# Optimization experiments

Measured on AMD Instinct MI355X. Metric: run time of the kernel, lower is better.

The kernel has to match this reference:

```python
import jax, jax.numpy as jnp
import numpy as np

NEG_SLOPE = 0.2  # PyG GATConv default negative_slope


def _gat(x, src, dst, N, W, a_src, a_dst, b, heads, ch, concat):
    # x: [N, F_in]; src/dst: [E] (self-loops already appended)
    h = (x @ W).reshape(N, heads, ch)                      # [N,H,C]
    s = jnp.sum(h * a_src, axis=-1)                        # [N,H]
    d = jnp.sum(h * a_dst, axis=-1)                        # [N,H]
    e = jax.nn.leaky_relu(s[src] + d[dst], NEG_SLOPE)      # [E,H]
    # segment softmax over incoming edges of each dst node
    m = jax.ops.segment_max(e, dst, num_segments=N)        # [N,H]
    ex = jnp.exp(e - m[dst])
    den = jax.ops.segment_sum(ex, dst, num_segments=N)     # [N,H]
    alpha = ex / den[dst]                                  # [E,H]
    out = jax.ops.segment_sum(h[src] * alpha[:, :, None], dst, num_segments=N)  # [N,H,C]
    out = out.reshape(N, heads * ch) if concat else out.mean(axis=1)
    return out + b


def setup_inputs() -> dict:
    key = jax.random.key(0)
    ks = jax.random.split(key, 20)
    N, E, F_in, H, C = 50000, 400000, 64, 4, 128
    x = jax.random.normal(ks[0], (N, F_in), dtype=jnp.float32)
    edge_index = jax.random.randint(ks[1], (2, E), 0, N, dtype=jnp.int64)

    def lin(k, fi, fo):
        return jax.random.normal(k, (fi, fo), dtype=jnp.float32) / np.float32(np.sqrt(fi))

    def att(k, h, c):
        return jax.random.normal(k, (h, c), dtype=jnp.float32) / np.float32(np.sqrt(c))

    return {
        "x": x, "edge_index": edge_index,
        "W1": lin(ks[2], F_in, H * C), "as1": att(ks[3], H, C), "ad1": att(ks[4], H, C), "b1": jnp.zeros((H * C,), jnp.float32),
        "W2": lin(ks[5], H * C, H * C), "as2": att(ks[6], H, C), "ad2": att(ks[7], H, C), "b2": jnp.zeros((H * C,), jnp.float32),
        "W3": lin(ks[8], H * C, C), "as3": att(ks[9], 1, C), "ad3": att(ks[10], 1, C), "b3": jnp.zeros((C,), jnp.float32),
        "cW1": lin(ks[11], C, C // 2), "cb1": jnp.zeros((C // 2,), jnp.float32),
        "cW2": lin(ks[12], C // 2, 2), "cb2": jnp.zeros((2,), jnp.float32),
    }


def reference(x, edge_index, W1, as1, ad1, b1, W2, as2, ad2, b2, W3, as3, ad3, b3, cW1, cb1, cW2, cb2):
    N = x.shape[0]
    loops = jnp.arange(N, dtype=edge_index.dtype)
    src = jnp.concatenate([edge_index[0], loops])
    dst = jnp.concatenate([edge_index[1], loops])
    h = _gat(x, src, dst, N, W1, as1, ad1, b1, 4, 128, True)
    h = jax.nn.relu(h)                         # dropout is identity at eval
    h = _gat(h, src, dst, N, W2, as2, ad2, b2, 4, 128, True)
    h = jax.nn.relu(h)
    h = _gat(h, src, dst, N, W3, as3, ad3, b3, 1, 128, False)
    out = jax.nn.relu(h @ cW1 + cb1) @ cW2 + cb2
    return jax.nn.log_softmax(out, axis=-1)
```

## Files before the change

### kernel.cpp

```cpp
#include <hip/hip_runtime.h>
#include <math.h>

#define NEG_SLOPE 0.2f

typedef __attribute__((ext_vector_type(8))) short short8;
typedef __attribute__((ext_vector_type(4))) float f32x4;
typedef unsigned short ushort_t;
typedef unsigned int u32;
typedef __attribute__((ext_vector_type(8))) unsigned short ushort8;
typedef __attribute__((ext_vector_type(4))) unsigned short ushort4v;

__device__ inline ushort_t f2bf(float f) {
    unsigned int u = __builtin_bit_cast(unsigned int, f);
    u += 0x7fffu + ((u >> 16) & 1u);
    return (ushort_t)(u >> 16);
}
__device__ inline float bf2f(ushort_t u) {
    unsigned int v = ((unsigned int)u) << 16;
    return __builtin_bit_cast(float, v);
}

__device__ inline void gl_lds16(const ushort_t* g, ushort_t* l) {
    __builtin_amdgcn_global_load_lds((const __attribute__((address_space(1))) u32*)g,
                                     (__attribute__((address_space(3))) u32*)l, 16, 0, 0);
}

__device__ inline int xcd_swizzle(int id, int nwg) {
    int q = nwg >> 3, r = nwg & 7;
    int xcd = id & 7, j = id >> 3;
    return (xcd < r ? xcd * (q + 1) : r * (q + 1) + (xcd - r) * q) + j;
}


__global__ void convert_count_kernel(const int* __restrict__ ei, int E, int N,
                                     int* __restrict__ deg,
                                     const float* __restrict__ x, ushort_t* __restrict__ xb, int n4x,
                                     const float* __restrict__ W1, ushort_t* __restrict__ W1t,
                                     const float* __restrict__ W2, ushort_t* __restrict__ W2t,
                                     const float* __restrict__ W3, ushort_t* __restrict__ W3t,
                                     const float* __restrict__ cW1, ushort_t* __restrict__ cW1t,
                                     const float* __restrict__ as1, const float* __restrict__ ad1,
                                     float* __restrict__ W1as, float* __restrict__ W1ad) {
    int i = blockIdx.x * blockDim.x + threadIdx.x;
    if (i < E + N) {
        int d = (i < E) ? ei[E + i] : (i - E);
        atomicAdd(&deg[d], 1);
    }
    if (i < n4x) {
        float4 v = ((const float4*)x)[i];
        ushort4v o;
        o.x = f2bf(v.x); o.y = f2bf(v.y); o.z = f2bf(v.z); o.w = f2bf(v.w);
        ((ushort4v*)xb)[i] = o;
        return;
    }
    int j = i - n4x;
    if (j < 64 * 512) {
        int k = j / 512, nn = j % 512;
        W1t[(size_t)nn * 64 + k] = f2bf(W1[j]);
        return;
    }
    j -= 64 * 512;
    if (j < 512 * 512) {
        int k = j / 512, nn = j % 512;
        W2t[(size_t)nn * 512 + k] = f2bf(W2[j]);
        return;
    }
    j -= 512 * 512;
    if (j < 512 * 128) {
        int k = j / 128, nn = j % 128;
        W3t[(size_t)nn * 512 + k] = f2bf(W3[j]);
        return;
    }
    j -= 512 * 128;
    if (j < 128 * 64) {
        int k = j / 64, nn = j % 64;
        cW1t[(size_t)nn * 128 + k] = f2bf(cW1[j]);
        return;
    }
    j -= 128 * 64;
    if (j < 512) {
        int k = j >> 3;
        int idx = j & 7;
        int h = idx & 3;
        int sel = idx >> 2;
        const float* av = sel ? ad1 : as1;
        float* outw = sel ? W1ad : W1as;
        const float* wrow = W1 + (size_t)k * 512 + h * 128;
        const float* arow = av + h * 128;
        float acc = 0.f;
        for (int c = 0; c < 128; c++) acc += wrow[c] * arow[c];
        outw[k * 4 + h] = acc;
    }
}

__global__ void scan1_kernel(const int* __restrict__ deg, int* __restrict__ rowptr,
                             int* __restrict__ bsum, int N) {
    __shared__ int sdata[256];
    int t = threadIdx.x;
    int base = blockIdx.x * 1024 + t * 4;
    int v[4];
#pragma unroll
    for (int k = 0; k < 4; k++) v[k] = (base + k < N) ? deg[base + k] : 0;
    int s = v[0] + v[1] + v[2] + v[3];
    sdata[t] = s;
    __syncthreads();
    for (int off = 1; off < 256; off <<= 1) {
        int x = (t >= off) ? sdata[t - off] : 0;
        __syncthreads();
        sdata[t] += x;
        __syncthreads();
    }
    int p = sdata[t] - s;
    if (t == 255) bsum[blockIdx.x] = sdata[255];
#pragma unroll
    for (int k = 0; k < 4; k++) {
        if (base + k < N) rowptr[base + k] = p;
        p += v[k];
    }
}

__global__ void scan2_kernel(int* __restrict__ bsum, int* __restrict__ rowptr, int nb, int N) {
    __shared__ int sh[256];
    int t = threadIdx.x;
    int v = (t < nb) ? bsum[t] : 0;
    sh[t] = v;
    __syncthreads();
    for (int off = 1; off < 256; off <<= 1) {
        int x = (t >= off) ? sh[t - off] : 0;
        __syncthreads();
        sh[t] += x;
        __syncthreads();
    }
    if (t < nb) bsum[t] = sh[t] - v;
    if (t == 255) rowptr[N] = sh[255];
}

__global__ void scan3_kernel(const int* __restrict__ bsum, int* __restrict__ rowptr,
                             int* __restrict__ cursor, int N) {
    int i = blockIdx.x * blockDim.x + threadIdx.x;
    if (i < N) {
        int v = rowptr[i] + bsum[i >> 10];
        rowptr[i] = v;
        cursor[i] = v;
    }
}

__global__ void fill_csr_kernel(const int* __restrict__ ei, int E, int N,
                                int* __restrict__ cursor, int* __restrict__ srcS) {
    int e = blockIdx.x * blockDim.x + threadIdx.x;
    if (e >= E + N) return;
    int s, d;
    if (e < E) { s = ei[e]; d = ei[E + e]; }
    else       { s = e - E; d = e - E; }
    int pos = atomicAdd(&cursor[d], 1);
    srcS[pos] = s;
}


__global__ __launch_bounds__(256) void score1_kernel(const ushort_t* __restrict__ xb,
                                                     const float* __restrict__ W1as,
                                                     const float* __restrict__ W1ad,
                                                     float* __restrict__ sOut,
                                                     float* __restrict__ dOut, int N) {
    __shared__ float wa[256];
    __shared__ float wd[256];
    int t = threadIdx.x;
    wa[t] = W1as[t];
    wd[t] = W1ad[t];
    __syncthreads();
    int n = blockIdx.x * 256 + t;
    if (n >= N) return;
    const ushort_t* xr = xb + (size_t)n * 64;
    float s_[4] = {0.f, 0.f, 0.f, 0.f};
    float d_[4] = {0.f, 0.f, 0.f, 0.f};
#pragma unroll
    for (int k8 = 0; k8 < 8; k8++) {
        ushort8 xv = *(const ushort8*)(xr + k8 * 8);
#pragma unroll
        for (int kk = 0; kk < 8; kk++) {
            float xf = bf2f(xv[kk]);
            int k = k8 * 8 + kk;
#pragma unroll
            for (int h = 0; h < 4; h++) {
                s_[h] += xf * wa[k * 4 + h];
                d_[h] += xf * wd[k * 4 + h];
            }
        }
    }
#pragma unroll
    for (int h = 0; h < 4; h++) {
        sOut[(size_t)n * 4 + h] = s_[h];
        dOut[(size_t)n * 4 + h] = d_[h];
    }
}


__global__ void agg1x_kernel(const ushort_t* __restrict__ xb, const float* __restrict__ s,
                             const float* __restrict__ dv, const int* __restrict__ rowptr,
                             const int* __restrict__ srcS, ushort_t* __restrict__ outp, int N) {
    int c = threadIdx.x & 31;
    int slot = threadIdx.x >> 5;
    int n = blockIdx.x * 8 + slot;
    if (n >= N) return;
    int h = c >> 3;
    int d8 = c & 7;
    float dn = dv[(size_t)n * 4 + h];
    int beg = rowptr[n], end = rowptr[n + 1];
    float acc[8] = {0.f, 0.f, 0.f, 0.f, 0.f, 0.f, 0.f, 0.f};
    float den = 0.f;
    for (int cb = beg; cb < end; cb += 8) {
        int j = cb + d8;
        int svg = 0;
        float al = 0.f;
        if (j < end) {
            svg = srcS[j];
            float e = s[(size_t)svg * 4 + h] + dn;
            e = (e >= 0.f) ? e : NEG_SLOPE * e;
            al = expf(fminf(e, 80.f));
        }
        int kmax = end - cb;
        if (kmax > 8) kmax = 8;
        for (int q = 0; q < kmax; q++) {
            float a = __shfl(al, h * 8 + q, 32);
            int sq = __shfl(svg, q, 32);
            den += a;
            ushort8 xv = *(const ushort8*)(xb + (size_t)sq * 64 + d8 * 8);
#pragma unroll
            for (int kk = 0; kk < 8; kk++) acc[kk] += a * bf2f(xv[kk]);
        }
    }
    float inv = 1.f / den;
    ushort8 o;
#pragma unroll
    for (int kk = 0; kk < 8; kk++) o[kk] = f2bf(acc[kk] * inv);
    ((ushort8*)outp)[(size_t)n * 32 + c] = o;
}


__global__ __launch_bounds__(256, 2) void tgemm1_kernel(
    const ushort_t* __restrict__ A, const ushort_t* __restrict__ Bt,
    const float* __restrict__ bias, ushort_t* __restrict__ C, int M) {
    __shared__ ushort_t As[128 * 32];
    __shared__ ushort_t Bs[128 * 32];
    int wg = xcd_swizzle(blockIdx.x, gridDim.x);
    int bm = (wg >> 2) * 128;
    int head = wg & 3;
    int bn = head * 128;
    int tid = threadIdx.x;
    int w = tid >> 6, lane = tid & 63;
    int wy = w >> 1, wx = w & 1;
    int r = lane & 15, quad = lane >> 4;
    int srow = lane >> 2;
    int scol = (lane & 3) * 8;
    f32x4 acc[4][4] = {};
    for (int k0 = 0; k0 < 64; k0 += 32) {
#pragma unroll
        for (int it = 0; it < 2; it++) {
            int rowb = w * 32 + it * 16;
            gl_lds16(A  + (size_t)(bm + rowb + srow) * 256 + head * 64 + k0 + scol, As + rowb * 32);
            gl_lds16(Bt + (size_t)(bn + rowb + srow) * 64 + k0 + scol, Bs + rowb * 32);
        }
        __syncthreads();
        short8 af[4], bfr[4];
#pragma unroll
        for (int i = 0; i < 4; i++)
            af[i] = *(const short8*)(As + (wy * 64 + i * 16 + r) * 32 + quad * 8);
#pragma unroll
        for (int j = 0; j < 4; j++)
            bfr[j] = *(const short8*)(Bs + (wx * 64 + j * 16 + r) * 32 + quad * 8);
#pragma unroll
        for (int i = 0; i < 4; i++)
#pragma unroll
            for (int j = 0; j < 4; j++)
                acc[i][j] = __builtin_amdgcn_mfma_f32_16x16x32_bf16(af[i], bfr[j], acc[i][j], 0, 0, 0);
        __syncthreads();
    }
#pragma unroll
    for (int i = 0; i < 4; i++) {
        int rowb = bm + wy * 64 + i * 16 + quad * 4;
#pragma unroll
        for (int j = 0; j < 4; j++) {
            int col = bn + wx * 64 + j * 16 + r;
            float bv = bias[col];
#pragma unroll
            for (int reg = 0; reg < 4; reg++) {
                int row = rowb + reg;
                if (row < M) C[(size_t)row * 512 + col] = f2bf(fmaxf(acc[i][j][reg] + bv, 0.f));
            }
        }
    }
}


template <bool SCORES>
__global__ __launch_bounds__(256, 2) void gemm_bf16_kernel(
    const ushort_t* __restrict__ A, const ushort_t* __restrict__ Bt,
    ushort_t* __restrict__ C,
    const float* __restrict__ a_s, const float* __restrict__ a_d,
    float* __restrict__ sOut, float* __restrict__ dOut, int H,
    int M, int Ncols, int K, int nbx) {
    __shared__ ushort_t As[128 * 32];
    __shared__ ushort_t Bs[128 * 32];
    __shared__ float sL[2][128];
    __shared__ float dL[2][128];
    int wg = xcd_swizzle(blockIdx.x, gridDim.x);
    int bm = (wg / nbx) * 128, bn = (wg % nbx) * 128;
    int tid = threadIdx.x;
    int w = tid >> 6, lane = tid & 63;
    int wy = w >> 1, wx = w & 1;
    int r = lane & 15, quad = lane >> 4;
    int srow = lane >> 2;
    int scol = (lane & 3) * 8;
    f32x4 acc[4][4] = {};
    for (int k0 = 0; k0 < K; k0 += 32) {
#pragma unroll
        for (int it = 0; it < 2; it++) {
            int rowb = w * 32 + it * 16;
            gl_lds16(A  + (size_t)(bm + rowb + srow) * K + k0 + scol, As + rowb * 32);
            gl_lds16(Bt + (size_t)(bn + rowb + srow) * K + k0 + scol, Bs + rowb * 32);
        }
        __syncthreads();
        short8 af[4], bfr[4];
#pragma unroll
        for (int i = 0; i < 4; i++)
            af[i] = *(const short8*)(As + (wy * 64 + i * 16 + r) * 32 + quad * 8);
#pragma unroll
        for (int j = 0; j < 4; j++)
            bfr[j] = *(const short8*)(Bs + (wx * 64 + j * 16 + r) * 32 + quad * 8);
#pragma unroll
        for (int i = 0; i < 4; i++)
#pragma unroll
            for (int j = 0; j < 4; j++)
                acc[i][j] = __builtin_amdgcn_mfma_f32_16x16x32_bf16(af[i], bfr[j], acc[i][j], 0, 0, 0);
        __syncthreads();
    }
#pragma unroll
    for (int i = 0; i < 4; i++) {
        int rowb = bm + wy * 64 + i * 16 + quad * 4;
#pragma unroll
        for (int j = 0; j < 4; j++) {
            int col = bn + wx * 64 + j * 16 + r;
            if (col >= Ncols) continue;
#pragma unroll
            for (int reg = 0; reg < 4; reg++) {
                int row = rowb + reg;
                if (row < M) C[(size_t)row * Ncols + col] = f2bf(acc[i][j][reg]);
            }
        }
    }
    if (SCORES) {
        int head = bn >> 7;
        float av[4], bv[4];
#pragma unroll
        for (int j = 0; j < 4; j++) {
            int c = wx * 64 + j * 16 + r;
            av[j] = a_s[head * 128 + c];
            bv[j] = a_d[head * 128 + c];
        }
#pragma unroll
        for (int i = 0; i < 4; i++) {
#pragma unroll
            for (int reg = 0; reg < 4; reg++) {
                float ps = acc[i][0][reg] * av[0] + acc[i][1][reg] * av[1]
                         + acc[i][2][reg] * av[2] + acc[i][3][reg] * av[3];
                float pd = acc[i][0][reg] * bv[0] + acc[i][1][reg] * bv[1]
                         + acc[i][2][reg] * bv[2] + acc[i][3][reg] * bv[3];
#pragma unroll
                for (int off = 8; off >= 1; off >>= 1) {
                    ps += __shfl_down(ps, off, 16);
                    pd += __shfl_down(pd, off, 16);
                }
                if (r == 0) {
                    int row128 = wy * 64 + i * 16 + quad * 4 + reg;
                    sL[wx][row128] = ps;
                    dL[wx][row128] = pd;
                }
            }
        }
        __syncthreads();
        if (tid < 128) {
            int row = bm + tid;
            if (row < M) {
                sOut[(size_t)row * H + head] = sL[0][tid] + sL[1][tid];
                dOut[(size_t)row * H + head] = dL[0][tid] + dL[1][tid];
            }
        }
    }
}


template <int HC, bool RELU>
__global__ void agg_fused_kernel(const ushort_t* __restrict__ h, const float* __restrict__ s,
                                 const float* __restrict__ dv, const int* __restrict__ rowptr,
                                 const int* __restrict__ srcS, const float* __restrict__ bias,
                                 ushort_t* __restrict__ outp, int N, int H) {
    const int TPN = HC / 8;
    const int NPB = 256 / TPN;
    int n = blockIdx.x * NPB + threadIdx.x / TPN;
    int c8 = threadIdx.x % TPN;
    if (n >= N) return;
    int head = (c8 * 8) >> 7;
    int g = c8 & 15;
    float dn = dv[(size_t)n * H + head];
    int beg = rowptr[n], end = rowptr[n + 1];
    float acc0[8] = {0.f, 0.f, 0.f, 0.f, 0.f, 0.f, 0.f, 0.f};
    float acc1[8] = {0.f, 0.f, 0.f, 0.f, 0.f, 0.f, 0.f, 0.f};
    float den = 0.f;
    for (int cb = beg; cb < end; cb += 16) {
        int je = cb + g;
        int svg = 0;
        float al = 0.f;
        if (je < end) {
            svg = srcS[je];
            float e = s[(size_t)svg * H + head] + dn;
            e = (e >= 0.f) ? e : NEG_SLOPE * e;
            al = expf(fminf(e, 80.f));
        }
        int kmax = end - cb;
        if (kmax > 16) kmax = 16;
        int k = 0;
        for (; k + 4 <= kmax; k += 4) {
            float a0 = __shfl(al, k, 16),     a1 = __shfl(al, k + 1, 16);
            float a2 = __shfl(al, k + 2, 16), a3 = __shfl(al, k + 3, 16);
            int s0 = __shfl(svg, k, 16),      s1 = __shfl(svg, k + 1, 16);
            int s2 = __shfl(svg, k + 2, 16),  s3 = __shfl(svg, k + 3, 16);
            den += a0 + a1 + a2 + a3;
            ushort8 hv0 = *(const ushort8*)(h + (size_t)s0 * HC + c8 * 8);
            ushort8 hv1 = *(const ushort8*)(h + (size_t)s1 * HC + c8 * 8);
            ushort8 hv2 = *(const ushort8*)(h + (size_t)s2 * HC + c8 * 8);
            ushort8 hv3 = *(const ushort8*)(h + (size_t)s3 * HC + c8 * 8);
#pragma unroll
            for (int kk = 0; kk < 8; kk++) {
                acc0[kk] += a0 * bf2f(hv0[kk]) + a2 * bf2f(hv2[kk]);
                acc1[kk] += a1 * bf2f(hv1[kk]) + a3 * bf2f(hv3[kk]);
            }
        }
        for (; k < kmax; k++) {
            float a0 = __shfl(al, k, 16);
            int s0 = __shfl(svg, k, 16);
            den += a0;
            ushort8 hv0 = *(const ushort8*)(h + (size_t)s0 * HC + c8 * 8);
#pragma unroll
            for (int kk = 0; kk < 8; kk++) acc0[kk] += a0 * bf2f(hv0[kk]);
        }
    }
    float inv = 1.f / den;
    float4 bv0 = ((const float4*)bias)[c8 * 2];
    float4 bv1 = ((const float4*)bias)[c8 * 2 + 1];
    float r[8];
#pragma unroll
    for (int k = 0; k < 8; k++) r[k] = (acc0[k] + acc1[k]) * inv;
    r[0] += bv0.x; r[1] += bv0.y; r[2] += bv0.z; r[3] += bv0.w;
    r[4] += bv1.x; r[5] += bv1.y; r[6] += bv1.z; r[7] += bv1.w;
    if (RELU) {
#pragma unroll
        for (int k = 0; k < 8; k++) r[k] = fmaxf(r[k], 0.f);
    }
    ushort8 o;
#pragma unroll
    for (int k = 0; k < 8; k++) o[k] = f2bf(r[k]);
    ((ushort8*)outp)[(size_t)n * TPN + c8] = o;
}


__global__ __launch_bounds__(256, 2) void cls_fused_kernel(
    const ushort_t* __restrict__ A, const ushort_t* __restrict__ Bt,
    const float* __restrict__ cb1, const float* __restrict__ cW2,
    const float* __restrict__ cb2, float* __restrict__ out, int M) {
    __shared__ ushort_t As[128 * 32];
    __shared__ ushort_t Bs[128 * 32];
    __shared__ float l0L[128];
    __shared__ float l1L[128];
    int wg = xcd_swizzle(blockIdx.x, gridDim.x);
    int bm = wg * 128;
    int tid = threadIdx.x;
    int w = tid >> 6, lane = tid & 63;
    int wy = w >> 1, wx = w & 1;
    int r = lane & 15, quad = lane >> 4;
    int srow = lane >> 2;
    int scol = (lane & 3) * 8;
    const int K = 128;
    f32x4 acc[4][4] = {};
    for (int k0 = 0; k0 < K; k0 += 32) {
#pragma unroll
        for (int it = 0; it < 2; it++) {
            int rowb = w * 32 + it * 16;
            gl_lds16(A  + (size_t)(bm + rowb + srow) * K + k0 + scol, As + rowb * 32);
            gl_lds16(Bt + (size_t)(rowb + srow) * K + k0 + scol, Bs + rowb * 32);
        }
        __syncthreads();
        short8 af[4], bfr[4];
#pragma unroll
        for (int i = 0; i < 4; i++)
            af[i] = *(const short8*)(As + (wy * 64 + i * 16 + r) * 32 + quad * 8);
#pragma unroll
        for (int j = 0; j < 4; j++)
            bfr[j] = *(const short8*)(Bs + (wx * 64 + j * 16 + r) * 32 + quad * 8);
#pragma unroll
        for (int i = 0; i < 4; i++)
#pragma unroll
            for (int j = 0; j < 4; j++)
                acc[i][j] = __builtin_amdgcn_mfma_f32_16x16x32_bf16(af[i], bfr[j], acc[i][j], 0, 0, 0);
        __syncthreads();
    }
    if (wx == 0) {
        float c1v[4], w20[4], w21[4];
#pragma unroll
        for (int j = 0; j < 4; j++) {
            int c = j * 16 + r;
            c1v[j] = cb1[c];
            w20[j] = cW2[c * 2];
            w21[j] = cW2[c * 2 + 1];
        }
#pragma unroll
        for (int i = 0; i < 4; i++) {
#pragma unroll
            for (int reg = 0; reg < 4; reg++) {
                float ps = 0.f, pd = 0.f;
#pragma unroll
                for (int j = 0; j < 4; j++) {
                    float v = fmaxf(acc[i][j][reg] + c1v[j], 0.f);
                    ps += v * w20[j];
                    pd += v * w21[j];
                }
#pragma unroll
                for (int off = 8; off >= 1; off >>= 1) {
                    ps += __shfl_down(ps, off, 16);
                    pd += __shfl_down(pd, off, 16);
                }
                if (r == 0) {
                    int row128 = wy * 64 + i * 16 + quad * 4 + reg;
                    l0L[row128] = ps;
                    l1L[row128] = pd;
                }
            }
        }
    }
    __syncthreads();
    if (tid < 128) {
        int row = bm + tid;
        if (row < M) {
            float l0 = l0L[tid] + cb2[0];
            float l1 = l1L[tid] + cb2[1];
            float mm = fmaxf(l0, l1);
            float lse = mm + logf(expf(l0 - mm) + expf(l1 - mm));
            out[(size_t)row * 2 + 0] = l0 - lse;
            out[(size_t)row * 2 + 1] = l1 - lse;
        }
    }
}


extern "C" void kernel_launch(void* const* d_in, const int* in_sizes, int n_in,
                              void* d_out, int out_size, void* d_ws, size_t ws_size,
                              hipStream_t stream) {
    const float* x   = (const float*)d_in[0];
    const int*   ei  = (const int*)d_in[1];
    const float* W1  = (const float*)d_in[2];
    const float* as1 = (const float*)d_in[3];
    const float* ad1 = (const float*)d_in[4];
    const float* b1  = (const float*)d_in[5];
    const float* W2  = (const float*)d_in[6];
    const float* as2 = (const float*)d_in[7];
    const float* ad2 = (const float*)d_in[8];
    const float* b2  = (const float*)d_in[9];
    const float* W3  = (const float*)d_in[10];
    const float* as3 = (const float*)d_in[11];
    const float* ad3 = (const float*)d_in[12];
    const float* b3  = (const float*)d_in[13];
    const float* cW1 = (const float*)d_in[14];
    const float* cb1 = (const float*)d_in[15];
    const float* cW2 = (const float*)d_in[16];
    const float* cb2 = (const float*)d_in[17];
    float* outp = (float*)d_out;

    const int N  = in_sizes[0] / 64;
    const int E  = in_sizes[1] / 2;
    const int E2 = E + N;
    const int NB = (N + 1023) / 1024;
    const int n4x = N * 16;

    char* ws = (char*)d_ws;
    size_t off = 0;
    auto alloc = [&](size_t bytes) -> void* {
        void* p = ws + off;
        off += (bytes + 255) & ~(size_t)255;
        return p;
    };
    ushort_t* Ab     = (ushort_t*)alloc((size_t)N * 512 * 2);
    ushort_t* Bb     = (ushort_t*)alloc((size_t)N * 512 * 2);
    ushort_t* xb     = (ushort_t*)alloc((size_t)N * 64 * 2);
    ushort_t* W1t    = (ushort_t*)alloc((size_t)512 * 64 * 2);
    ushort_t* W2t    = (ushort_t*)alloc((size_t)512 * 512 * 2);
    ushort_t* W3t    = (ushort_t*)alloc((size_t)128 * 512 * 2);
    ushort_t* cW1t   = (ushort_t*)alloc((size_t)128 * 128 * 2);
    float*    W1as   = (float*)alloc((size_t)64 * 4 * 4);
    float*    W1ad   = (float*)alloc((size_t)64 * 4 * 4);
    float*    sbuf   = (float*)alloc((size_t)N * 4 * 4);
    float*    dbuf   = (float*)alloc((size_t)N * 4 * 4);
    int*      srcS   = (int*)alloc((size_t)E2 * 4);
    int*      deg    = (int*)alloc((size_t)N * 4);
    int*      cursor = (int*)alloc((size_t)N * 4);
    int*      rowptr = (int*)alloc((size_t)(N + 1) * 4);
    int*      bsum   = (int*)alloc((size_t)256 * 4);
    (void)ws_size; (void)n_in; (void)out_size;

    hipMemsetAsync(deg, 0, (size_t)N * 4, stream);
    {
        int tot = n4x + 64 * 512 + 512 * 512 + 512 * 128 + 128 * 64 + 512;
        if (E2 > tot) tot = E2;
        convert_count_kernel<<<(tot + 255) / 256, 256, 0, stream>>>(
            ei, E, N, deg, x, xb, n4x, W1, W1t, W2, W2t, W3, W3t, cW1, cW1t,
            as1, ad1, W1as, W1ad);
    }
    scan1_kernel<<<NB, 256, 0, stream>>>(deg, rowptr, bsum, N);
    scan2_kernel<<<1, 256, 0, stream>>>(bsum, rowptr, NB, N);
    scan3_kernel<<<(N + 255) / 256, 256, 0, stream>>>(bsum, rowptr, cursor, N);
    fill_csr_kernel<<<(E2 + 255) / 256, 256, 0, stream>>>(ei, E, N, cursor, srcS);

    dim3 gB(256);
    const int mt = (N + 127) / 128;
    const int g512 = 4 * mt;
    const int g128 = mt;

    score1_kernel<<<(N + 255) / 256, 256, 0, stream>>>(xb, W1as, W1ad, sbuf, dbuf, N);
    agg1x_kernel<<<(N + 7) / 8, 256, 0, stream>>>(xb, sbuf, dbuf, rowptr, srcS, Ab, N);
    tgemm1_kernel<<<g512, gB, 0, stream>>>(Ab, W1t, b1, Bb, N);

    gemm_bf16_kernel<true><<<g512, gB, 0, stream>>>(
        Bb, W2t, Ab, as2, ad2, sbuf, dbuf, 4, N, 512, 512, 4);
    agg_fused_kernel<512, true><<<(N + 3) / 4, 256, 0, stream>>>(
        Ab, sbuf, dbuf, rowptr, srcS, b2, Bb, N, 4);

    gemm_bf16_kernel<true><<<g128, gB, 0, stream>>>(
        Bb, W3t, Ab, as3, ad3, sbuf, dbuf, 1, N, 128, 512, 1);
    agg_fused_kernel<128, false><<<(N + 15) / 16, 256, 0, stream>>>(
        Ab, sbuf, dbuf, rowptr, srcS, b3, Bb, N, 1);

    cls_fused_kernel<<<g128, gB, 0, stream>>>(Bb, cW1t, cb1, cW2, cb2, outp, N);
}
```

Before: 373.8 us.

## Use 64-wide K tiles with XOR-swizzled LDS layout in bf16 GEMMs

```diff
diff --git a/kernel.cpp b/kernel.cpp
--- a/kernel.cpp
+++ b/kernel.cpp
@@ -29,6 +29,10 @@
     int q = nwg >> 3, r = nwg & 7;
     int xcd = id & 7, j = id >> 3;
     return (xcd < r ? xcd * (q + 1) : r * (q + 1) + (xcd - r) * q) + j;
+}
+
+__device__ inline int swz_us(int row, int colb) {
+    return row * 64 + ((colb ^ ((row & 7) << 4)) >> 1);
 }
 
 
@@ -240,8 +244,8 @@
 __global__ __launch_bounds__(256, 2) void tgemm1_kernel(
     const ushort_t* __restrict__ A, const ushort_t* __restrict__ Bt,
     const float* __restrict__ bias, ushort_t* __restrict__ C, int M) {
-    __shared__ ushort_t As[128 * 32];
-    __shared__ ushort_t Bs[128 * 32];
+    __shared__ ushort_t As[128 * 64];
+    __shared__ ushort_t Bs[128 * 64];
     int wg = xcd_swizzle(blockIdx.x, gridDim.x);
     int bm = (wg >> 2) * 128;
     int head = wg & 3;
@@ -250,30 +254,31 @@
     int w = tid >> 6, lane = tid & 63;
     int wy = w >> 1, wx = w & 1;
     int r = lane & 15, quad = lane >> 4;
-    int srow = lane >> 2;
-    int scol = (lane & 3) * 8;
+    int srow = lane >> 3;
+    int scol = ((lane & 7) ^ srow) << 3;
     f32x4 acc[4][4] = {};
-    for (int k0 = 0; k0 < 64; k0 += 32) {
-#pragma unroll
-        for (int it = 0; it < 2; it++) {
-            int rowb = w * 32 + it * 16;
-            gl_lds16(A  + (size_t)(bm + rowb + srow) * 256 + head * 64 + k0 + scol, As + rowb * 32);
-            gl_lds16(Bt + (size_t)(bn + rowb + srow) * 64 + k0 + scol, Bs + rowb * 32);
-        }
-        __syncthreads();
+#pragma unroll
+    for (int it = 0; it < 4; it++) {
+        int rowb = it * 32 + w * 8;
+        gl_lds16(A  + (size_t)(bm + rowb + srow) * 256 + head * 64 + scol, As + rowb * 64);
+        gl_lds16(Bt + (size_t)(bn + rowb + srow) * 64 + scol, Bs + rowb * 64);
+    }
+    __syncthreads();
+#pragma unroll
+    for (int kh = 0; kh < 2; kh++) {
         short8 af[4], bfr[4];
+        int colb = kh * 64 + quad * 16;
 #pragma unroll
         for (int i = 0; i < 4; i++)
-            af[i] = *(const short8*)(As + (wy * 64 + i * 16 + r) * 32 + quad * 8);
+            af[i] = *(const short8*)(As + swz_us(wy * 64 + i * 16 + r, colb));
 #pragma unroll
         for (int j = 0; j < 4; j++)
-            bfr[j] = *(const short8*)(Bs + (wx * 64 + j * 16 + r) * 32 + quad * 8);
+            bfr[j] = *(const short8*)(Bs + swz_us(wx * 64 + j * 16 + r, colb));
 #pragma unroll
         for (int i = 0; i < 4; i++)
 #pragma unroll
             for (int j = 0; j < 4; j++)
                 acc[i][j] = __builtin_amdgcn_mfma_f32_16x16x32_bf16(af[i], bfr[j], acc[i][j], 0, 0, 0);
-        __syncthreads();
     }
 #pragma unroll
     for (int i = 0; i < 4; i++) {
@@ -299,8 +304,8 @@
     const float* __restrict__ a_s, const float* __restrict__ a_d,
     float* __restrict__ sOut, float* __restrict__ dOut, int H,
     int M, int Ncols, int K, int nbx) {
-    __shared__ ushort_t As[128 * 32];
-    __shared__ ushort_t Bs[128 * 32];
+    __shared__ ushort_t As[128 * 64];
+    __shared__ ushort_t Bs[128 * 64];
     __shared__ float sL[2][128];
     __shared__ float dL[2][128];
     int wg = xcd_swizzle(blockIdx.x, gridDim.x);
@@ -309,29 +314,33 @@
     int w = tid >> 6, lane = tid & 63;
     int wy = w >> 1, wx = w & 1;
     int r = lane & 15, quad = lane >> 4;
-    int srow = lane >> 2;
-    int scol = (lane & 3) * 8;
+    int srow = lane >> 3;
+    int scol = ((lane & 7) ^ srow) << 3;
     f32x4 acc[4][4] = {};
-    for (int k0 = 0; k0 < K; k0 += 32) {
-#pragma unroll
-        for (int it = 0; it < 2; it++) {
-            int rowb = w * 32 + it * 16;
-            gl_lds16(A  + (size_t)(bm + rowb + srow) * K + k0 + scol, As + rowb * 32);
-            gl_lds16(Bt + (size_t)(bn + rowb + srow) * K + k0 + scol, Bs + rowb * 32);
-        }
-        __syncthreads();
-        short8 af[4], bfr[4];
-#pragma unroll
-        for (int i = 0; i < 4; i++)
-            af[i] = *(const short8*)(As + (wy * 64 + i * 16 + r) * 32 + quad * 8);
-#pragma unroll
-        for (int j = 0; j < 4; j++)
-            bfr[j] = *(const short8*)(Bs + (wx * 64 + j * 16 + r) * 32 + quad * 8);
-#pragma unroll
-        for (int i = 0; i < 4; i++)
+    for (int k0 = 0; k0 < K; k0 += 64) {
+#pragma unroll
+        for (int it = 0; it < 4; it++) {
+            int rowb = it * 32 + w * 8;
+            gl_lds16(A  + (size_t)(bm + rowb + srow) * K + k0 + scol, As + rowb * 64);
+            gl_lds16(Bt + (size_t)(bn + rowb + srow) * K + k0 + scol, Bs + rowb * 64);
+        }
+        __syncthreads();
+#pragma unroll
+        for (int kh = 0; kh < 2; kh++) {
+            short8 af[4], bfr[4];
+            int colb = kh * 64 + quad * 16;
+#pragma unroll
+            for (int i = 0; i < 4; i++)
+                af[i] = *(const short8*)(As + swz_us(wy * 64 + i * 16 + r, colb));
 #pragma unroll
             for (int j = 0; j < 4; j++)
-                acc[i][j] = __builtin_amdgcn_mfma_f32_16x16x32_bf16(af[i], bfr[j], acc[i][j], 0, 0, 0);
+                bfr[j] = *(const short8*)(Bs + swz_us(wx * 64 + j * 16 + r, colb));
+#pragma unroll
+            for (int i = 0; i < 4; i++)
+#pragma unroll
+                for (int j = 0; j < 4; j++)
+                    acc[i][j] = __builtin_amdgcn_mfma_f32_16x16x32_bf16(af[i], bfr[j], acc[i][j], 0, 0, 0);
+        }
         __syncthreads();
     }
 #pragma unroll
@@ -467,8 +476,8 @@
     const ushort_t* __restrict__ A, const ushort_t* __restrict__ Bt,
     const float* __restrict__ cb1, const float* __restrict__ cW2,
     const float* __restrict__ cb2, float* __restrict__ out, int M) {
-    __shared__ ushort_t As[128 * 32];
-    __shared__ ushort_t Bs[128 * 32];
+    __shared__ ushort_t As[128 * 64];
+    __shared__ ushort_t Bs[128 * 64];
     __shared__ float l0L[128];
     __shared__ float l1L[128];
     int wg = xcd_swizzle(blockIdx.x, gridDim.x);
@@ -477,30 +486,34 @@
     int w = tid >> 6, lane = tid & 63;
     int wy = w >> 1, wx = w & 1;
     int r = lane & 15, quad = lane >> 4;
-    int srow = lane >> 2;
-    int scol = (lane & 3) * 8;
+    int srow = lane >> 3;
+    int scol = ((lane & 7) ^ srow) << 3;
     const int K = 128;
     f32x4 acc[4][4] = {};
-    for (int k0 = 0; k0 < K; k0 += 32) {
-#pragma unroll
-        for (int it = 0; it < 2; it++) {
-            int rowb = w * 32 + it * 16;
-            gl_lds16(A  + (size_t)(bm + rowb + srow) * K + k0 + scol, As + rowb * 32);
-            gl_lds16(Bt + (size_t)(rowb + srow) * K + k0 + scol, Bs + rowb * 32);
-        }
-        __syncthreads();
-        short8 af[4], bfr[4];
-#pragma unroll
-        for (int i = 0; i < 4; i++)
-            af[i] = *(const short8*)(As + (wy * 64 + i * 16 + r) * 32 + quad * 8);
-#pragma unroll
-        for (int j = 0; j < 4; j++)
-            bfr[j] = *(const short8*)(Bs + (wx * 64 + j * 16 + r) * 32 + quad * 8);
-#pragma unroll
-        for (int i = 0; i < 4; i++)
+    for (int k0 = 0; k0 < K; k0 += 64) {
+#pragma unroll
+        for (int it = 0; it < 4; it++) {
+            int rowb = it * 32 + w * 8;
+            gl_lds16(A  + (size_t)(bm + rowb + srow) * K + k0 + scol, As + rowb * 64);
+            gl_lds16(Bt + (size_t)(rowb + srow) * K + k0 + scol, Bs + rowb * 64);
+        }
+        __syncthreads();
+#pragma unroll
+        for (int kh = 0; kh < 2; kh++) {
+            short8 af[4], bfr[4];
+            int colb = kh * 64 + quad * 16;
+#pragma unroll
+            for (int i = 0; i < 4; i++)
+                af[i] = *(const short8*)(As + swz_us(wy * 64 + i * 16 + r, colb));
 #pragma unroll
             for (int j = 0; j < 4; j++)
-                acc[i][j] = __builtin_amdgcn_mfma_f32_16x16x32_bf16(af[i], bfr[j], acc[i][j], 0, 0, 0);
+                bfr[j] = *(const short8*)(Bs + swz_us(wx * 64 + j * 16 + r, colb));
+#pragma unroll
+            for (int i = 0; i < 4; i++)
+#pragma unroll
+                for (int j = 0; j < 4; j++)
+                    acc[i][j] = __builtin_amdgcn_mfma_f32_16x16x32_bf16(af[i], bfr[j], acc[i][j], 0, 0, 0);
+        }
         __syncthreads();
     }
     if (wx == 0) {
```

Measured after the change: 366.2 us, median of 2. 1.02x faster.
